# Optimization experiments

Measured on AMD Instinct MI355X. Metric: run time of the kernel, lower is better.

Reference implementation:

```python
import jax, jax.numpy as jnp
import numpy as np

DIM = 1024
HEADS = 16
DIM_HEAD = 64
INNER = HEADS * DIM_HEAD  # 1024
SCALE = DIM_HEAD ** -0.5


def setup_inputs() -> dict:
    key = jax.random.key(0)
    ks = jax.random.split(key, 7)
    b, n = 4, 1024
    x = jax.random.normal(ks[0], (b, n, DIM), dtype=jnp.float32)
    # Dense kernels (glorot-ish scale), mix-head matrices are N(0,1) as in source
    Wq = jax.random.normal(ks[1], (DIM, INNER), dtype=jnp.float32) * (DIM ** -0.5)
    Wkv = jax.random.normal(ks[2], (DIM, 2 * INNER), dtype=jnp.float32) * (DIM ** -0.5)
    mix_pre = jax.random.normal(ks[3], (HEADS, HEADS), dtype=jnp.float32)
    mix_post = jax.random.normal(ks[4], (HEADS, HEADS), dtype=jnp.float32)
    Wo = jax.random.normal(ks[5], (INNER, DIM), dtype=jnp.float32) * (INNER ** -0.5)
    bo = jnp.zeros((DIM,), dtype=jnp.float32)
    return {"x": x, "Wq": Wq, "Wkv": Wkv, "mix_pre": mix_pre,
            "mix_post": mix_post, "Wo": Wo, "bo": bo}


def reference(x, Wq, Wkv, mix_pre, mix_post, Wo, bo):
    b, n, _ = x.shape
    # context = x (self-attention path)
    q = x @ Wq                      # [b, n, inner]
    kv = x @ Wkv                    # [b, n, 2*inner]
    k, v = jnp.split(kv, 2, axis=-1)
    split_heads = lambda t: t.reshape(b, n, HEADS, DIM_HEAD).transpose(0, 2, 1, 3)
    q, k, v = map(split_heads, (q, k, v))  # [b, h, n, d]
    dots = jnp.einsum('bhid,bhjd->bhij', q, k) * SCALE
    dots = jnp.einsum('bhij,hg->bgij', dots, mix_pre)   # talking-heads pre-softmax
    attn = jax.nn.softmax(dots, axis=-1)
    attn = jnp.einsum('bhij,hg->bgij', attn, mix_post)  # talking-heads post-softmax
    out = jnp.einsum('bhij,bhjd->bhid', attn, v)        # [b, h, n, d]
    out = out.transpose(0, 2, 1, 3).reshape(b, n, INNER)
    return out @ Wo + bo            # dropout rate 0 -> identity
```

## Files before the change

### kernel.cpp

```cpp
#include <hip/hip_runtime.h>
#include <hip/hip_bf16.h>

using bf16 = __hip_bfloat16;

typedef __bf16 bf16x8 __attribute__((ext_vector_type(8)));
typedef __bf16 bf16x2v __attribute__((ext_vector_type(2)));
typedef float  f32x4  __attribute__((ext_vector_type(4)));
typedef float  f32x2  __attribute__((ext_vector_type(2)));

#define QK_SCALE 0.125f

__device__ __forceinline__ void load_lds16(const bf16* g, bf16* l) {
  __builtin_amdgcn_global_load_lds(
      (const __attribute__((address_space(1))) unsigned int*)g,
      (__attribute__((address_space(3))) unsigned int*)l, 16, 0, 0);
}

__device__ __forceinline__ unsigned pack_bf2(float a, float b) {
  bf16x2v v;
  v[0] = (__bf16)a;
  v[1] = (__bf16)b;
  return __builtin_bit_cast(unsigned, v);
}

struct alignas(8) bf16x4s { bf16 a, b, c, d; };
__global__ void f32_to_bf16_k(const float4* __restrict__ in, bf16x4s* __restrict__ out, int n4)
{
  const int i = blockIdx.x * blockDim.x + threadIdx.x;
  if (i < n4) {
    const float4 v = in[i];
    out[i] = { (bf16)v.x, (bf16)v.y, (bf16)v.z, (bf16)v.w };
  }
}

template<int TM, int TN, int WM, int WN, bool BIAS, typename CT>
__global__ __launch_bounds__(256, 2)
void gemm_nt(const bf16* __restrict__ A, const bf16* __restrict__ B,
             CT* __restrict__ C, const float* __restrict__ bias,
             int K, int lda, int ldb, int ldc,
             long sA0, long sA1, long sB0, long sB1, long sC0, long sC1,
             int nz1, float alpha)
{
  constexpr int BK = 64;
  constexpr int LDE = TN + 8;
  constexpr unsigned SB_STAGE = (TM + TN) * BK * 2;
  constexpr unsigned SB_EP = (sizeof(CT) == 2) ? TM * LDE * 2 : 0;
  constexpr unsigned SBYTES = SB_STAGE > SB_EP ? SB_STAGE : SB_EP;
  __shared__ __align__(16) char smem[SBYTES];
  bf16* lsA = (bf16*)smem;
  bf16* lsB = lsA + TM * BK;

  const int z = blockIdx.z;
  A += (long)(z / nz1) * sA0 + (long)(z % nz1) * sA1;
  B += (long)(z / nz1) * sB0 + (long)(z % nz1) * sB1;
  C += (long)(z / nz1) * sC0 + (long)(z % nz1) * sC1;
  const int tm0 = blockIdx.y * TM;
  const int tn0 = blockIdx.x * TN;

  const int tid = threadIdx.x;
  const int w = tid >> 6, l = tid & 63;
  constexpr int WCOLS = TN / WN;
  const int wm = (w / WCOLS) * WM, wn = (w % WCOLS) * WN;
  constexpr int AM = WM / 16, AN = WN / 16;
  f32x4 acc[AM][AN] = {};
  const int kg = l >> 4, rl = l & 15;

  constexpr int RA = TM / 32, RB = TN / 32;
  const int srow0 = tid >> 3;
  const int schunk = tid & 7;

  for (int k0 = 0; k0 < K; k0 += BK) {
#pragma unroll
    for (int r = 0; r < RA; ++r) {
      const int row = r * 32 + srow0;
      const int sw = ((row >> 1) & 7) ^ ((row & 1) << 2);
      const int col8 = schunk ^ sw;
      load_lds16(A + (long)(tm0 + row) * lda + (k0 + col8 * 8),
                 &lsA[row * BK + schunk * 8]);
    }
#pragma unroll
    for (int r = 0; r < RB; ++r) {
      const int row = r * 32 + srow0;
      const int sw = ((row >> 1) & 7) ^ ((row & 1) << 2);
      const int col8 = schunk ^ sw;
      load_lds16(B + (long)(tn0 + row) * ldb + (k0 + col8 * 8),
                 &lsB[row * BK + schunk * 8]);
    }
    __syncthreads();

#pragma unroll
    for (int half = 0; half < 2; ++half) {
      bf16x8 af[AM], bfr[AN];
#pragma unroll
      for (int i = 0; i < AM; ++i) {
        const int m = wm + i * 16 + rl;
        const int sw = ((m >> 1) & 7) ^ ((m & 1) << 2);
        const int p = (half * 4 + kg) ^ sw;
        af[i] = *(const bf16x8*)&lsA[m * BK + p * 8];
      }
#pragma unroll
      for (int j = 0; j < AN; ++j) {
        const int n = wn + j * 16 + rl;
        const int sw = ((n >> 1) & 7) ^ ((n & 1) << 2);
        const int p = (half * 4 + kg) ^ sw;
        bfr[j] = *(const bf16x8*)&lsB[n * BK + p * 8];
      }
#pragma unroll
      for (int i = 0; i < AM; ++i)
#pragma unroll
        for (int j = 0; j < AN; ++j)
          acc[i][j] = __builtin_amdgcn_mfma_f32_16x16x32_bf16(af[i], bfr[j], acc[i][j], 0, 0, 0);
    }
    __syncthreads();
  }

  if constexpr (sizeof(CT) == 2) {
    bf16* ep = (bf16*)smem;
#pragma unroll
    for (int i = 0; i < AM; ++i) {
#pragma unroll
      for (int j = 0; j < AN; ++j) {
        const int col = wn + j * 16 + rl;
        float bv = 0.f;
        if (BIAS) bv = bias[tn0 + col];
#pragma unroll
        for (int v = 0; v < 4; ++v) {
          const int row = wm + i * 16 + (l >> 4) * 4 + v;
          ep[row * LDE + col] = (bf16)(acc[i][j][v] * alpha + bv);
        }
      }
    }
    __syncthreads();
    constexpr int CH = (TM * TN) / 2048;
#pragma unroll
    for (int c = 0; c < CH; ++c) {
      const int gidx = (c * 256 + tid) * 8;
      const int row = gidx / TN, col = gidx % TN;
      *(uint4*)&C[(long)(tm0 + row) * ldc + tn0 + col] = *(const uint4*)&ep[row * LDE + col];
    }
  } else {
#pragma unroll
    for (int i = 0; i < AM; ++i) {
#pragma unroll
      for (int j = 0; j < AN; ++j) {
        const int col = tn0 + wn + j * 16 + rl;
        float bv = 0.f;
        if (BIAS) bv = bias[col];
#pragma unroll
        for (int v = 0; v < 4; ++v) {
          const int row = tm0 + wm + i * 16 + (l >> 4) * 4 + v;
          C[(long)row * ldc + col] = (CT)(acc[i][j][v] * alpha + bv);
        }
      }
    }
  }
}

template<typename TI>
__global__ void transpose_k(const TI* __restrict__ in, bf16* __restrict__ out,
                            int ldi, int ldo,
                            long sI0, long sI1, long sO0, long sO1, int nz1)
{
  __shared__ bf16 t[32][33];
  const int z = blockIdx.z;
  in  += (long)(z / nz1) * sI0 + (long)(z % nz1) * sI1;
  out += (long)(z / nz1) * sO0 + (long)(z % nz1) * sO1;
  const int c0 = blockIdx.x * 32, r0 = blockIdx.y * 32;
  const int x = threadIdx.x, y = threadIdx.y;
#pragma unroll
  for (int dy = 0; dy < 32; dy += 8)
    t[y + dy][x] = (bf16)(float)in[(long)(r0 + y + dy) * ldi + c0 + x];
  __syncthreads();
#pragma unroll
  for (int dy = 0; dy < 32; dy += 8)
    out[(long)(c0 + y + dy) * ldo + r0 + x] = t[x][y + dy];
}

__global__ __launch_bounds__(256)
void mix_softmax_mix(bf16* __restrict__ S,
                     const float* __restrict__ mixpre, const float* __restrict__ mixpost)
{
  constexpr int LDJ = 1028;
  __shared__ __align__(16) unsigned int lSp[8 * LDJ];
  __shared__ float pre[256], post[256];
  __shared__ float redZ[4][16];
  const int i = blockIdx.x, b = blockIdx.y;
  const int tid = threadIdx.x;
  pre[tid]  = mixpre[tid];
  post[tid] = mixpost[tid];
  const long hstr = 1048576L;
  bf16* Srow = S + (long)b * 16 * hstr + (long)i * 1024;
  const int w = tid >> 6, l = tid & 63;
  const int rl = l & 15, q = l >> 4;

#pragma unroll
  for (int r = 0; r < 4; ++r) {
    const int u = r * 256 + tid;
    const int h2 = u >> 7, jg = (u & 127) * 8;
    const uint4 a  = *(const uint4*)&Srow[(long)(2 * h2)     * hstr + jg];
    const uint4 c4 = *(const uint4*)&Srow[(long)(2 * h2 + 1) * hstr + jg];
    uint4 w0, w1;
    w0.x = (a.x & 0xFFFFu) | (c4.x << 16);
    w0.y = (a.x >> 16)     | (c4.x & 0xFFFF0000u);
    w0.z = (a.y & 0xFFFFu) | (c4.y << 16);
    w0.w = (a.y >> 16)     | (c4.y & 0xFFFF0000u);
    w1.x = (a.z & 0xFFFFu) | (c4.z << 16);
    w1.y = (a.z >> 16)     | (c4.z & 0xFFFF0000u);
    w1.z = (a.w & 0xFFFFu) | (c4.w << 16);
    w1.w = (a.w >> 16)     | (c4.w & 0xFFFF0000u);
    *(uint4*)&lSp[h2 * LDJ + jg]     = w0;
    *(uint4*)&lSp[h2 * LDJ + jg + 4] = w1;
  }
  __syncthreads();

  bf16x8 aHi, aLo;
#pragma unroll
  for (int e = 0; e < 8; ++e) {
    const int h = q * 8 + e;
    const float c = (h < 16) ? pre[(h & 15) * 16 + rl] : 0.f;
    const __bf16 hi = (__bf16)c;
    aHi[e] = hi;
    aLo[e] = (__bf16)(c - (float)hi);
  }

  const int hq2 = (q & 1) * 4;
  const int cw = w * 256;

  unsigned ph01[16], ph23[16];
  f32x4 zac = {0.f, 0.f, 0.f, 0.f};
#pragma unroll
  for (int c = 0; c < 16; ++c) {
    const int col = cw + c * 16 + rl;
    uint4 bw;
    bw.x = lSp[(hq2 + 0) * LDJ + col];
    bw.y = lSp[(hq2 + 1) * LDJ + col];
    bw.z = lSp[(hq2 + 2) * LDJ + col];
    bw.w = lSp[(hq2 + 3) * LDJ + col];
    const bf16x8 bfr = __builtin_bit_cast(bf16x8, bw);
    f32x4 d = __builtin_amdgcn_mfma_f32_16x16x32_bf16(aHi, bfr, f32x4{0.f,0.f,0.f,0.f}, 0, 0, 0);
    d = __builtin_amdgcn_mfma_f32_16x16x32_bf16(aLo, bfr, d, 0, 0, 0);
    float ev[4];
#pragma unroll
    for (int v = 0; v < 4; ++v) {
      ev[v] = __expf(d[v] - 10.f);
      zac[v] += ev[v];
    }
    ph01[c] = pack_bf2(ev[0], ev[1]);
    ph23[c] = pack_bf2(ev[2], ev[3]);
  }
#pragma unroll
  for (int off = 1; off < 16; off <<= 1) {
#pragma unroll
    for (int v = 0; v < 4; ++v) zac[v] += __shfl_xor(zac[v], off, 64);
  }
  if (rl == 0) {
#pragma unroll
    for (int v = 0; v < 4; ++v) redZ[w][q * 4 + v] = zac[v];
  }
  __syncthreads();

  bf16x8 pHi, pLo;
#pragma unroll
  for (int e = 0; e < 8; ++e) {
    const int g = q * 8 + e;
    float c = 0.f;
    if (g < 16) {
      const float Z = redZ[0][g & 15] + redZ[1][g & 15] + redZ[2][g & 15] + redZ[3][g & 15];
      c = post[(g & 15) * 16 + rl] / Z;
    }
    const __bf16 hi = (__bf16)c;
    pHi[e] = hi;
    pLo[e] = (__bf16)(c - (float)hi);
  }

  const int src0 = rl + 32 * (q & 1);
  const int src1 = src0 + 16;
#pragma unroll
  for (int c = 0; c < 16; ++c) {
    const unsigned d0 = (unsigned)__shfl((int)ph01[c], src0, 64);
    const unsigned d1 = (unsigned)__shfl((int)ph23[c], src0, 64);
    const unsigned d2 = (unsigned)__shfl((int)ph01[c], src1, 64);
    const unsigned d3 = (unsigned)__shfl((int)ph23[c], src1, 64);
    uint4 raw = {d0, d1, d2, d3};
    bf16x8 bfr = *(const bf16x8*)&raw;
    f32x4 d = __builtin_amdgcn_mfma_f32_16x16x32_bf16(pHi, bfr, f32x4{0.f,0.f,0.f,0.f}, 0, 0, 0);
    d = __builtin_amdgcn_mfma_f32_16x16x32_bf16(pLo, bfr, d, 0, 0, 0);
    const int col = cw + c * 16 + rl;
#pragma unroll
    for (int v = 0; v < 4; ++v)
      Srow[(long)(q * 4 + v) * hstr + col] = (bf16)d[v];
  }
}

extern "C" void kernel_launch(void* const* d_in, const int* in_sizes, int n_in,
                              void* d_out, int out_size, void* d_ws, size_t ws_size,
                              hipStream_t stream)
{
  const float* x     = (const float*)d_in[0];
  const float* Wq    = (const float*)d_in[1];
  const float* Wkv   = (const float*)d_in[2];
  const float* mpre  = (const float*)d_in[3];
  const float* mpost = (const float*)d_in[4];
  const float* Wo    = (const float*)d_in[5];
  const float* bo    = (const float*)d_in[6];
  float* out = (float*)d_out;

  char* ws = (char*)d_ws;
  const size_t MB = 1024 * 1024;
  if (ws_size < 184 * MB) return;
  bf16* xb   = (bf16*)(ws);
  bf16* QKV  = (bf16*)(ws + 8 * MB);
  bf16* WT   = (bf16*)(ws + 32 * MB);
  bf16* WoT  = (bf16*)(ws + 38 * MB);
  bf16* VT   = (bf16*)(ws + 40 * MB);
  bf16* Obuf = (bf16*)(ws + 48 * MB);
  bf16* Sbuf = (bf16*)(ws + 56 * MB);

  const dim3 tb(32, 8, 1);

  f32_to_bf16_k<<<4096, 256, 0, stream>>>((const float4*)x, (bf16x4s*)xb, 1048576);

  transpose_k<float><<<dim3(32, 32, 1), tb, 0, stream>>>(Wq,  WT,           1024, 1024, 0, 0, 0, 0, 1);
  transpose_k<float><<<dim3(64, 32, 1), tb, 0, stream>>>(Wkv, WT + 1048576, 2048, 1024, 0, 0, 0, 0, 1);
  transpose_k<float><<<dim3(32, 32, 1), tb, 0, stream>>>(Wo,  WoT,          1024, 1024, 0, 0, 0, 0, 1);

  gemm_nt<128, 128, 64, 64, false, bf16><<<dim3(24, 32, 1), 256, 0, stream>>>(
      xb, WT, QKV, nullptr, 1024, 1024, 1024, 3072, 0, 0, 0, 0, 0, 0, 1, 1.f);

  transpose_k<bf16><<<dim3(2, 32, 64), tb, 0, stream>>>(
      QKV + 2048, VT, 3072, 1024,
      3145728, 64, 16L * 65536, 65536, 16);

  gemm_nt<128, 128, 64, 64, false, bf16><<<dim3(8, 8, 64), 256, 0, stream>>>(
      QKV, QKV + 1024, Sbuf, nullptr, 64, 3072, 3072, 1024,
      3145728, 64, 3145728, 64, 16L * 1048576, 1048576, 16, QK_SCALE);

  mix_softmax_mix<<<dim3(1024, 4, 1), 256, 0, stream>>>(Sbuf, mpre, mpost);

  gemm_nt<128, 64, 64, 32, false, bf16><<<dim3(1, 8, 64), 256, 0, stream>>>(
      Sbuf, VT, Obuf, nullptr, 1024, 1024, 1024, 1024,
      16L * 1048576, 1048576, 16L * 65536, 65536, 1048576, 64, 16, 1.f);

  gemm_nt<128, 128, 64, 64, true, float><<<dim3(8, 32, 1), 256, 0, stream>>>(
      Obuf, WoT, out, bo, 1024, 1024, 1024, 1024, 0, 0, 0, 0, 0, 0, 1, 1.f);
}
```

Baseline: 262.1 us.

## Fuse prep kernels and compute V transposed directly via GEMM

Merges the x conversion and the three weight transposes into one launch, dispatching on block index. The QKV GEMM now produces only Q and K. V^T is computed by a separate GEMM (Wv^T × x^T) that writes straight into the layout the PV GEMM expects, removing the strided bf16 transpose pass over V. This cuts kernel launches and one intermediate read/write, at the cost of an extra GEMM launch with a smaller tile shape.

```diff
diff --git a/kernel.cpp b/kernel.cpp
--- a/kernel.cpp
+++ b/kernel.cpp
@@ -24,13 +24,43 @@
 }
 
 struct alignas(8) bf16x4s { bf16 a, b, c, d; };
-__global__ void f32_to_bf16_k(const float4* __restrict__ in, bf16x4s* __restrict__ out, int n4)
+
+__global__ __launch_bounds__(256)
+void prep_k(const float* __restrict__ x, bf16x4s* __restrict__ xb,
+            const float* __restrict__ Wq, const float* __restrict__ Wkv,
+            const float* __restrict__ Wo,
+            bf16* __restrict__ WT, bf16* __restrict__ WoT)
 {
-  const int i = blockIdx.x * blockDim.x + threadIdx.x;
-  if (i < n4) {
-    const float4 v = in[i];
-    out[i] = { (bf16)v.x, (bf16)v.y, (bf16)v.z, (bf16)v.w };
-  }
+  const int bid = blockIdx.x;
+  const int tid = threadIdx.x;
+
+  if (bid >= 4096) {
+    const int i = (bid - 4096) * 256 + tid;
+    const float4 v = ((const float4*)x)[i];
+    xb[i] = { (bf16)v.x, (bf16)v.y, (bf16)v.z, (bf16)v.w };
+    return;
+  }
+
+  __shared__ bf16 t[32][33];
+  const float* in;
+  bf16* out;
+  int ldi, c0, r0;
+  if (bid < 1024)      { in = Wq;  out = WT;           ldi = 1024;
+                         c0 = (bid & 31) * 32;        r0 = (bid >> 5) * 32; }
+  else if (bid < 3072) { const int lb = bid - 1024;
+                         in = Wkv; out = WT + 1048576; ldi = 2048;
+                         c0 = (lb % 64) * 32;          r0 = (lb / 64) * 32; }
+  else                 { const int lb = bid - 3072;
+                         in = Wo;  out = WoT;          ldi = 1024;
+                         c0 = (lb & 31) * 32;          r0 = (lb >> 5) * 32; }
+  const int xx = tid & 31, yy = tid >> 5;
+#pragma unroll
+  for (int dy = 0; dy < 32; dy += 8)
+    t[yy + dy][xx] = (bf16)in[(long)(r0 + yy + dy) * ldi + c0 + xx];
+  __syncthreads();
+#pragma unroll
+  for (int dy = 0; dy < 32; dy += 8)
+    out[(long)(c0 + yy + dy) * 1024 + r0 + xx] = t[xx][yy + dy];
 }
 
 template<int TM, int TN, int WM, int WN, bool BIAS, typename CT>
@@ -156,26 +186,6 @@
   }
 }
 
-template<typename TI>
-__global__ void transpose_k(const TI* __restrict__ in, bf16* __restrict__ out,
-                            int ldi, int ldo,
-                            long sI0, long sI1, long sO0, long sO1, int nz1)
-{
-  __shared__ bf16 t[32][33];
-  const int z = blockIdx.z;
-  in  += (long)(z / nz1) * sI0 + (long)(z % nz1) * sI1;
-  out += (long)(z / nz1) * sO0 + (long)(z % nz1) * sO1;
-  const int c0 = blockIdx.x * 32, r0 = blockIdx.y * 32;
-  const int x = threadIdx.x, y = threadIdx.y;
-#pragma unroll
-  for (int dy = 0; dy < 32; dy += 8)
-    t[y + dy][x] = (bf16)(float)in[(long)(r0 + y + dy) * ldi + c0 + x];
-  __syncthreads();
-#pragma unroll
-  for (int dy = 0; dy < 32; dy += 8)
-    out[(long)(c0 + y + dy) * ldo + r0 + x] = t[x][y + dy];
-}
-
 __global__ __launch_bounds__(256)
 void mix_softmax_mix(bf16* __restrict__ S,
                      const float* __restrict__ mixpre, const float* __restrict__ mixpost)
@@ -316,20 +326,14 @@
   bf16* Obuf = (bf16*)(ws + 48 * MB);
   bf16* Sbuf = (bf16*)(ws + 56 * MB);
 
-  const dim3 tb(32, 8, 1);
-
-  f32_to_bf16_k<<<4096, 256, 0, stream>>>((const float4*)x, (bf16x4s*)xb, 1048576);
-
-  transpose_k<float><<<dim3(32, 32, 1), tb, 0, stream>>>(Wq,  WT,           1024, 1024, 0, 0, 0, 0, 1);
-  transpose_k<float><<<dim3(64, 32, 1), tb, 0, stream>>>(Wkv, WT + 1048576, 2048, 1024, 0, 0, 0, 0, 1);
-  transpose_k<float><<<dim3(32, 32, 1), tb, 0, stream>>>(Wo,  WoT,          1024, 1024, 0, 0, 0, 0, 1);
-
-  gemm_nt<128, 128, 64, 64, false, bf16><<<dim3(24, 32, 1), 256, 0, stream>>>(
+  prep_k<<<8192, 256, 0, stream>>>(x, (bf16x4s*)xb, Wq, Wkv, Wo, WT, WoT);
+
+  gemm_nt<128, 128, 64, 64, false, bf16><<<dim3(16, 32, 1), 256, 0, stream>>>(
       xb, WT, QKV, nullptr, 1024, 1024, 1024, 3072, 0, 0, 0, 0, 0, 0, 1, 1.f);
 
-  transpose_k<bf16><<<dim3(2, 32, 64), tb, 0, stream>>>(
-      QKV + 2048, VT, 3072, 1024,
-      3145728, 64, 16L * 65536, 65536, 16);
+  gemm_nt<64, 128, 32, 64, false, bf16><<<dim3(8, 1, 64), 256, 0, stream>>>(
+      WT + 2097152, xb, VT, nullptr, 1024, 1024, 1024, 1024,
+      0, 65536, 1048576, 0, 1048576, 65536, 16, 1.f);
 
   gemm_nt<128, 128, 64, 64, false, bf16><<<dim3(8, 8, 64), 256, 0, stream>>>(
       QKV, QKV + 1024, Sbuf, nullptr, 64, 3072, 3072, 1024,
```

Measured after the change: 259.8 us. About the same (-0.9%).
